# Kernel optimization log

Hardware: AMD Instinct MI355X
Metric: run time of the kernel (lower is better)

The kernel has to match this reference:

```python
import jax, jax.numpy as jnp
import numpy as np

B, T, C, H = 4, 2048, 1024, 16
HD = C // H  # head_dim = 64


def _rope(x, cos, sin):
    # x: [B,H,T,HD]; cos/sin: [T,HD//2] -> broadcast [1,1,T,HD//2]
    x1 = x[..., 0::2]
    x2 = x[..., 1::2]
    cos = cos[None, None]
    sin = sin[None, None]
    o1 = x1 * cos - x2 * sin
    o2 = x1 * sin + x2 * cos
    # interleave back to [..., HD]
    return jnp.stack([o1, o2], axis=-1).reshape(x.shape)


def setup_inputs() -> dict:
    key = jax.random.key(0)
    ks = jax.random.split(key, 10)
    x = jax.random.normal(ks[0], (B, T, C), jnp.float32)
    # rotary frequencies (llama-style, theta=10000), stored as (cos,sin)
    inv_freq = 1.0 / (10000.0 ** (jnp.arange(0, HD, 2, dtype=jnp.float32) / HD))
    freqs = jnp.outer(jnp.arange(T, dtype=jnp.float32), inv_freq)  # [T, HD/2]
    freqs_cis = jnp.stack([jnp.cos(freqs), jnp.sin(freqs)], axis=-1)  # [T, HD/2, 2]
    attn_mask = jnp.tril(jnp.ones((T, T), jnp.int32))  # causal
    padding_mask = jnp.ones((B, T), jnp.int32)
    w = 0.02
    Wq = jax.random.normal(ks[1], (C, C), jnp.float32) * w
    Wk = jax.random.normal(ks[2], (C, C), jnp.float32) * w
    Wv = jax.random.normal(ks[3], (C, C), jnp.float32) * w
    Wp = jax.random.normal(ks[4], (C, C), jnp.float32) * w
    bq = jnp.zeros((C,), jnp.float32)
    bk = jnp.zeros((C,), jnp.float32)
    bv = jnp.zeros((C,), jnp.float32)
    bp = jnp.zeros((C,), jnp.float32)
    return {"x": x, "freqs_cis": freqs_cis, "attn_mask": attn_mask,
            "padding_mask": padding_mask, "Wq": Wq, "bq": bq, "Wk": Wk,
            "bk": bk, "Wv": Wv, "bv": bv, "Wp": Wp, "bp": bp}


def reference(x, freqs_cis, attn_mask, padding_mask, Wq, bq, Wk, bk, Wv, bv, Wp, bp):
    b, t, c = x.shape
    # qkv projections -> [B,H,T,HD]
    def heads(y):
        return y.reshape(b, t, H, HD).transpose(0, 2, 1, 3)
    q = heads(x @ Wq.T + bq)
    k = heads(x @ Wk.T + bk)
    v = heads(x @ Wv.T + bv)
    cos, sin = freqs_cis[..., 0], freqs_cis[..., 1]  # [T, HD/2]
    q = _rope(q, cos, sin)
    k = _rope(k, cos, sin)
    att = jnp.einsum('bhqd,bhkd->bhqk', q, k) * (1.0 / np.sqrt(HD).astype(np.float32))
    att = jnp.where(attn_mask[None, None] == 0, -1e30, att)
    att = jnp.where(padding_mask[:, None, None, :] == 0, -1e30, att)
    att = jax.nn.softmax(att, axis=-1)
    # dropout omitted (eval mode / deterministic reference)
    y = jnp.einsum('bhqk,bhkd->bhqd', att, v)
    y = y.transpose(0, 2, 1, 3).reshape(b, t, c)
    return y @ Wp.T + bp
```

## Files before the change

kernel.cpp:

```cpp
#include <hip/hip_runtime.h>
#include <hip/hip_bf16.h>

#define TB 2048
#define CC 1024
#define NH 16
#define HD 64
#define NB 4
#define BHX (NB*NH)
#define BTX (NB*TB)
#define NITEMS 2048

typedef __attribute__((ext_vector_type(8))) short bf16x8;
typedef __attribute__((ext_vector_type(4))) float f32x4;
typedef __attribute__((ext_vector_type(4))) unsigned short us4;

__device__ __forceinline__ unsigned short bfb(float f) {
  __hip_bfloat16 h = __float2bfloat16(f);
  return __builtin_bit_cast(unsigned short, h);
}
__device__ __forceinline__ float fexp2(float x) {
  return __builtin_amdgcn_exp2f(x);
}
template <int CTRL>
__device__ __forceinline__ float dppf(float x) {
  int r = __builtin_amdgcn_update_dpp(0, __builtin_bit_cast(int, x), CTRL, 0xf, 0xf, false);
  return __builtin_bit_cast(float, r);
}

__device__ __forceinline__ void gld_lds16(const void* g, void* l) {
  __builtin_amdgcn_global_load_lds(
      (const __attribute__((address_space(1))) unsigned*)g,
      (__attribute__((address_space(3))) unsigned*)l, 16, 0, 0);
}

__global__ void cvt_f32_bf16(const float* __restrict__ src,
                             unsigned short* __restrict__ dst, int n4) {
  int i = blockIdx.x * blockDim.x + threadIdx.x;
  if (i >= n4) return;
  f32x4 v = ((const f32x4*)src)[i];
  us4 o;
#pragma unroll
  for (int j = 0; j < 4; j++) o[j] = bfb(v[j]);
  ((us4*)dst)[i] = o;
}

__global__ void cvt_w4(const float* __restrict__ s0, const float* __restrict__ s1,
                       const float* __restrict__ s2, const float* __restrict__ s3,
                       unsigned short* __restrict__ d0, unsigned short* __restrict__ d1,
                       unsigned short* __restrict__ d2, unsigned short* __restrict__ d3) {
  int y = blockIdx.y;
  const float* s = y == 0 ? s0 : y == 1 ? s1 : y == 2 ? s2 : s3;
  unsigned short* d = y == 0 ? d0 : y == 1 ? d1 : y == 2 ? d2 : d3;
  int i = blockIdx.x * 256 + threadIdx.x;
  f32x4 v = ((const f32x4*)s)[i];
  us4 o;
#pragma unroll
  for (int j = 0; j < 4; j++) o[j] = bfb(v[j]);
  ((us4*)d)[i] = o;
}

__global__ void prep_bias(const float* __restrict__ bq, const float* __restrict__ bk,
                          const float* __restrict__ bv, float* __restrict__ out) {
  int i = blockIdx.x * 256 + threadIdx.x;
  float v = i < 1024 ? bq[i] : i < 2048 ? bk[i - 1024] : bv[i - 2048];
  out[i] = v;
}

template <int MODE>
__global__ __launch_bounds__(256) void gemm_bt(
    const unsigned short* __restrict__ A, const unsigned short* __restrict__ Bw,
    const float* __restrict__ bias, const float* __restrict__ fcg,
    void* __restrict__ Cout, int M, int N, int K)
{
  __shared__ __align__(16) unsigned short As[128 * 32];
  __shared__ __align__(16) unsigned short Bs[128 * 32];
  int tid = threadIdx.x;
  int lane = tid & 63, wid = tid >> 6;
  int g = lane >> 4, l4 = lane & 15;
  int wr = wid >> 1, wc = wid & 1;
  int brow = blockIdx.y * 128, bcol = blockIdx.x * 128;

  const unsigned short* ap = A + (size_t)(brow + (tid >> 2)) * K + (tid & 3) * 8;
  const unsigned short* bp_ = Bw + (size_t)(bcol + (tid >> 2)) * K + (tid & 3) * 8;
  const size_t rstep = (size_t)64 * K;
  unsigned short* asl = As + tid * 8;
  unsigned short* bsl = Bs + tid * 8;

  f32x4 acc[4][4] = {};

  for (int k0 = 0; k0 < K; k0 += 32) {
    gld_lds16(ap, asl);
    gld_lds16(ap + rstep, asl + 2048);
    gld_lds16(bp_, bsl);
    gld_lds16(bp_ + rstep, bsl + 2048);
    ap += 32; bp_ += 32;
    __syncthreads();
    bf16x8 af[4], bfr[4];
#pragma unroll
    for (int i = 0; i < 4; i++)
      af[i] = *(const bf16x8*)&As[(wr * 64 + i * 16 + l4) * 32 + g * 8];
#pragma unroll
    for (int i = 0; i < 4; i++)
      bfr[i] = *(const bf16x8*)&Bs[(wc * 64 + i * 16 + l4) * 32 + g * 8];
#pragma unroll
    for (int i = 0; i < 4; i++)
#pragma unroll
      for (int j = 0; j < 4; j++)
        acc[i][j] = __builtin_amdgcn_mfma_f32_16x16x32_bf16(af[i], bfr[j], acc[i][j], 0, 0, 0);
    __syncthreads();
  }

#pragma unroll
  for (int i = 0; i < 4; i++) {
    int grow0 = brow + wr * 64 + i * 16 + 4 * g;
#pragma unroll
    for (int j = 0; j < 4; j++) {
      int gcol = bcol + wc * 64 + j * 16 + l4;
      float bv = bias[gcol];
      if (MODE == 0) {
        float* out = (float*)Cout;
#pragma unroll
        for (int r = 0; r < 4; r++)
          out[(size_t)(grow0 + r) * N + gcol] = acc[i][j][r] + bv;
      } else {
        unsigned short* out = (unsigned short*)Cout;
        int part = gcol >> 10;
        int c = gcol & 1023;
        int h = c >> 6, d = c & 63;
        int dbase = d & ~1;
        float sgn = (d & 1) ? 1.f : -1.f;
        bool isqk = (part < 2);
#pragma unroll
        for (int r = 0; r < 4; r++) {
          int grow = grow0 + r;
          int b = grow >> 11, t = grow & 2047;
          float v = acc[i][j][r] + bv;
          float w = __shfl_xor(v, 1, 64);
          float o = v;
          if (isqk) {
            float cth = fcg[(size_t)t * 64 + dbase];
            float sth = fcg[(size_t)t * 64 + dbase + 1];
            o = v * cth + sgn * w * sth;
          }
          size_t dst = (size_t)part * ((size_t)BHX * TB * HD)
                     + ((size_t)(b * NH + h) * TB + t) * HD + d;
          out[dst] = bfb(o);
        }
      }
    }
  }
}

__global__ void transpose_v(const unsigned short* __restrict__ v,
                            unsigned short* __restrict__ vT) {
  int bh = blockIdx.y, t0 = blockIdx.x * 64;
  __shared__ __align__(16) unsigned short tile[64][72];
  int tid = threadIdx.x;
#pragma unroll
  for (int s = 0; s < 2; s++) {
    int cid = tid + 256 * s;
    int r = cid >> 3, c8 = (cid & 7) * 8;
    bf16x8 val = *(const bf16x8*)(v + ((size_t)bh * TB + t0 + r) * HD + c8);
    *(bf16x8*)&tile[r][c8] = val;
  }
  __syncthreads();
#pragma unroll
  for (int s = 0; s < 2; s++) {
    int cid = tid + 256 * s;
    int rr = cid >> 3, cc = (cid & 7) * 8;
    bf16x8 o;
#pragma unroll
    for (int i = 0; i < 8; i++) o[i] = (short)tile[cc + i][rr];
    *(bf16x8*)(vT + ((size_t)bh * HD + rr) * TB + t0 + cc) = o;
  }
}

__global__ __launch_bounds__(256, 4) void flash_fwd(
    const unsigned short* __restrict__ q, const unsigned short* __restrict__ k,
    const unsigned short* __restrict__ vT, unsigned short* __restrict__ yb,
    int* __restrict__ ctr)
{
  __shared__ __align__(16) unsigned short Ks[2][4096];
  __shared__ __align__(16) unsigned short Vs[2][4096];
  __shared__ __align__(16) unsigned short Ps[4][16][64];

  const int tid = threadIdx.x, wid = tid >> 6, lane = tid & 63;
  const int g = lane >> 4, l4 = lane & 15;

  const int off0 = tid << 4;
  const int row0 = off0 >> 7, sc0 = ((off0 >> 4) & 7) ^ (row0 & 7);
  const int off1 = off0 + 4096;
  const int row1 = off1 >> 7, sc1 = ((off1 >> 4) & 7) ^ (row1 & 7);
  const int koff0 = (row0 << 6) + (sc0 << 3);
  const int koff1 = (row1 << 6) + (sc1 << 3);
  const int voff0 = (row0 << 11) + (sc0 << 3);
  const int voff1 = (row1 << 11) + (sc1 << 3);

  const float SCL2 = 0.18033688011112042f;

  for (;;) {
    __syncthreads();
    if (tid == 0) *(int*)&Ps[0][0][0] = atomicAdd(ctr, 1);
    __syncthreads();
    const int w = *(const int*)&Ps[0][0][0];
    if (w >= NITEMS) break;
    const int q64 = 31 - (w >> 6), bh = w & 63;
    const int rbase = q64 * 64 + wid * 16;

    const unsigned short* kb = k  + ((size_t)bh << 17);
    const unsigned short* vb = vT + ((size_t)bh << 17);

    bf16x8 qf0, qf1;
    {
      const unsigned short* qp = q + (((size_t)bh * TB + rbase + l4) << 6);
      qf0 = *(const bf16x8*)(qp + g * 8);
      qf1 = *(const bf16x8*)(qp + 32 + g * 8);
    }

    float m_run[4], l_run[4];
    f32x4 acc_o[4] = {};
#pragma unroll
    for (int j = 0; j < 4; j++) { m_run[j] = -1e30f; l_run[j] = 0.f; }

    gld_lds16(kb + koff0, &Ks[0][off0 >> 1]);
    gld_lds16(kb + koff1, &Ks[0][off1 >> 1]);
    gld_lds16(vb + voff0, &Vs[0][off0 >> 1]);
    gld_lds16(vb + voff1, &Vs[0][off1 >> 1]);
    __syncthreads();

    for (int kt = 0; kt <= q64; kt++) {
      const int cur = kt & 1;
      if (kt < q64) {
        const int kadd = (kt + 1) << 12;
        const int vadd = (kt + 1) << 6;
        gld_lds16(kb + koff0 + kadd, &Ks[cur ^ 1][off0 >> 1]);
        gld_lds16(kb + koff1 + kadd, &Ks[cur ^ 1][off1 >> 1]);
        gld_lds16(vb + voff0 + vadd, &Vs[cur ^ 1][off0 >> 1]);
        gld_lds16(vb + voff1 + vadd, &Vs[cur ^ 1][off1 >> 1]);
      }
      const unsigned short* Kc = Ks[cur];
      const unsigned short* Vc = Vs[cur];

      float sv[4][4];
      __builtin_amdgcn_s_setprio(1);
#pragma unroll
      for (int cb = 0; cb < 4; cb++) {
        const int r = cb * 16 + l4;
        const int sw = (r & 7) * 8;
        bf16x8 kb0 = *(const bf16x8*)&Kc[r * 64 + ((g * 8) ^ sw)];
        bf16x8 kb1 = *(const bf16x8*)&Kc[r * 64 + (((g + 4) * 8) ^ sw)];
        f32x4 z = {0.f, 0.f, 0.f, 0.f};
        z = __builtin_amdgcn_mfma_f32_16x16x32_bf16(qf0, kb0, z, 0, 0, 0);
        z = __builtin_amdgcn_mfma_f32_16x16x32_bf16(qf1, kb1, z, 0, 0, 0);
#pragma unroll
        for (int j = 0; j < 4; j++)
          sv[cb][j] = z[j] * SCL2;
      }
      __builtin_amdgcn_s_setprio(0);
      if (kt == q64) {
        const int rq = wid * 16 + 4 * g;
#pragma unroll
        for (int cb = 0; cb < 4; cb++)
#pragma unroll
          for (int j = 0; j < 4; j++)
            if (cb * 16 + l4 > rq + j) sv[cb][j] = -1e30f;
      }

      float mt[4];
#pragma unroll
      for (int j = 0; j < 4; j++) {
        float m = fmaxf(fmaxf(sv[0][j], sv[1][j]), fmaxf(sv[2][j], sv[3][j]));
        m = fmaxf(m, dppf<0x121>(m));
        m = fmaxf(m, dppf<0x122>(m));
        m = fmaxf(m, dppf<0x124>(m));
        m = fmaxf(m, dppf<0x128>(m));
        mt[j] = m;
      }
      bool need = !((mt[0] <= m_run[0] + 8.f) & (mt[1] <= m_run[1] + 8.f) &
                    (mt[2] <= m_run[2] + 8.f) & (mt[3] <= m_run[3] + 8.f));
      if (__any(need)) {
#pragma unroll
        for (int j = 0; j < 4; j++) {
          float mn = fmaxf(m_run[j], mt[j]);
          float alpha = fexp2(m_run[j] - mn);
          m_run[j] = mn;
          l_run[j] *= alpha;
#pragma unroll
          for (int db = 0; db < 4; db++) acc_o[db][j] *= alpha;
        }
      }
#pragma unroll
      for (int j = 0; j < 4; j++) {
        float s0 = fexp2(sv[0][j] - m_run[j]); sv[0][j] = s0;
        float s1 = fexp2(sv[1][j] - m_run[j]); sv[1][j] = s1;
        float s2 = fexp2(sv[2][j] - m_run[j]); sv[2][j] = s2;
        float s3 = fexp2(sv[3][j] - m_run[j]); sv[3][j] = s3;
        float p = (s0 + s1) + (s2 + s3);
        p += dppf<0x121>(p);
        p += dppf<0x122>(p);
        p += dppf<0x124>(p);
        p += dppf<0x128>(p);
        l_run[j] += p;
      }

#pragma unroll
      for (int cb = 0; cb < 4; cb++)
#pragma unroll
        for (int j = 0; j < 4; j++) {
          const int xch = (cb * 2 + (l4 >> 3)) ^ ((g & 1) * 4 + j);
          Ps[wid][4 * g + j][xch * 8 + (l4 & 7)] = bfb(sv[cb][j]);
        }
      asm volatile("s_waitcnt lgkmcnt(0)" ::: "memory");
      __builtin_amdgcn_sched_barrier(0);
      bf16x8 pa0 = *(const bf16x8*)&Ps[wid][l4][(g ^ (l4 & 7)) * 8];
      bf16x8 pa1 = *(const bf16x8*)&Ps[wid][l4][((4 + g) ^ (l4 & 7)) * 8];
      __builtin_amdgcn_s_setprio(1);
#pragma unroll
      for (int db = 0; db < 4; db++) {
        const int r = db * 16 + l4;
        const int sw = (r & 7) * 8;
        bf16x8 vb0 = *(const bf16x8*)&Vc[r * 64 + ((g * 8) ^ sw)];
        bf16x8 vb1 = *(const bf16x8*)&Vc[r * 64 + (((g + 4) * 8) ^ sw)];
        acc_o[db] = __builtin_amdgcn_mfma_f32_16x16x32_bf16(pa0, vb0, acc_o[db], 0, 0, 0);
        acc_o[db] = __builtin_amdgcn_mfma_f32_16x16x32_bf16(pa1, vb1, acc_o[db], 0, 0, 0);
      }
      __builtin_amdgcn_s_setprio(0);
      __syncthreads();
    }

    unsigned short* yp = yb + ((size_t)(bh >> 4) * TB) * CC + (size_t)(bh & 15) * HD;
    const int qr0 = rbase + 4 * g;
    float inv[4];
#pragma unroll
    for (int j = 0; j < 4; j++) inv[j] = 1.0f / l_run[j];
#pragma unroll
    for (int db = 0; db < 4; db++) {
      const int d = db * 16 + l4;
#pragma unroll
      for (int j = 0; j < 4; j++)
        yp[(size_t)(qr0 + j) * CC + d] = bfb(acc_o[db][j] * inv[j]);
    }
  }
}

extern "C" void kernel_launch(void* const* d_in, const int* in_sizes, int n_in,
                              void* d_out, int out_size, void* d_ws, size_t ws_size,
                              hipStream_t stream) {
  (void)in_sizes; (void)n_in; (void)out_size; (void)ws_size;
  const float* x  = (const float*)d_in[0];
  const float* fc = (const float*)d_in[1];
  const float* Wq = (const float*)d_in[4];
  const float* bq = (const float*)d_in[5];
  const float* Wk = (const float*)d_in[6];
  const float* bk = (const float*)d_in[7];
  const float* Wv = (const float*)d_in[8];
  const float* bv = (const float*)d_in[9];
  const float* Wp = (const float*)d_in[10];
  const float* bp = (const float*)d_in[11];

  char* ws = (char*)d_ws;
  unsigned short* xb   = (unsigned short*)(ws + 0);
  unsigned short* wqkv = (unsigned short*)(ws + 16777216);
  unsigned short* wp   = (unsigned short*)(ws + 23068672);
  float*          bqkv = (float*)(ws + 25165824);
  int*            ctr  = (int*)(ws + 25178112);
  unsigned short* qkv  = (unsigned short*)(ws + 25182208);
  unsigned short* vT   = qkv + 3 * (size_t)8388608;
  unsigned short* yb   = xb;

  cvt_f32_bf16<<<(2097152 + 255) / 256, 256, 0, stream>>>(x, xb, 2097152);
  cvt_w4<<<dim3(1024, 4), 256, 0, stream>>>(Wq, Wk, Wv, Wp,
      wqkv, wqkv + 1048576, wqkv + 2097152, wp);
  prep_bias<<<dim3(12), 256, 0, stream>>>(bq, bk, bv, bqkv);
  (void)hipMemsetAsync(ctr, 0, 4, stream);

  gemm_bt<1><<<dim3(24, 64), 256, 0, stream>>>(xb, wqkv, bqkv, fc, qkv, BTX, 3072, 1024);
  transpose_v<<<dim3(32, 64), 256, 0, stream>>>(qkv + 2 * (size_t)8388608, vT);
  flash_fwd<<<dim3(1024), 256, 0, stream>>>(qkv, qkv + (size_t)8388608, vT, yb, ctr);
  gemm_bt<0><<<dim3(8, 64), 256, 0, stream>>>(yb, wp, bp, nullptr, (float*)d_out, BTX, 1024, 1024);
}
```

Measured before the change: 246.6 us.

## Partition flash attention work queue per XCD with global work-stealing fallback

Replaces the single global atomic work counter with per-XCD counters, so each XCD first processes items whose heads map to it (bh low bits from the XCD id). K/V for those heads then stay in that XCD's L2. Once a local queue is exhausted, blocks steal from a global counter, and a claimed-flag array prevents duplicate work. This adds more atomics per item and a larger memset. The item order within each XCD still runs the longest causal rows first.

```diff
diff --git a/kernel.cpp b/kernel.cpp
--- a/kernel.cpp
+++ b/kernel.cpp
@@ -178,7 +178,7 @@
 __global__ __launch_bounds__(256, 4) void flash_fwd(
     const unsigned short* __restrict__ q, const unsigned short* __restrict__ k,
     const unsigned short* __restrict__ vT, unsigned short* __restrict__ yb,
-    int* __restrict__ ctr)
+    int* __restrict__ ctrs, int* __restrict__ claimed)
 {
   __shared__ __align__(16) unsigned short Ks[2][4096];
   __shared__ __align__(16) unsigned short Vs[2][4096];
@@ -186,6 +186,10 @@
 
   const int tid = threadIdx.x, wid = tid >> 6, lane = tid & 63;
   const int g = lane >> 4, l4 = lane & 15;
+
+  int xcd;
+  asm("s_getreg_b32 %0, hwreg(HW_REG_XCC_ID)" : "=s"(xcd));
+  xcd &= 7;
 
   const int off0 = tid << 4;
   const int row0 = off0 >> 7, sc0 = ((off0 >> 4) & 7) ^ (row0 & 7);
@@ -198,13 +202,34 @@
 
   const float SCL2 = 0.18033688011112042f;
 
+  bool own = true;
   for (;;) {
     __syncthreads();
-    if (tid == 0) *(int*)&Ps[0][0][0] = atomicAdd(ctr, 1);
+    if (tid == 0) {
+      int item;
+      if (own) {
+        int it = atomicAdd(&ctrs[xcd], 1);
+        if (it < 256) {
+          item = (xcd << 8) | it;
+          if (atomicExch(&claimed[item], 1)) item = -3;
+        } else item = -2;
+      } else {
+        item = -1;
+        for (;;) {
+          int it = atomicAdd(&ctrs[8], 1);
+          if (it >= NITEMS) break;
+          if (atomicExch(&claimed[it], 1) == 0) { item = it; break; }
+        }
+      }
+      *(int*)&Ps[0][0][0] = item;
+    }
     __syncthreads();
-    const int w = *(const int*)&Ps[0][0][0];
-    if (w >= NITEMS) break;
-    const int q64 = 31 - (w >> 6), bh = w & 63;
+    const int item = *(const int*)&Ps[0][0][0];
+    if (item == -3) continue;
+    if (item == -2) { own = false; continue; }
+    if (item < 0) break;
+    const int bh = ((item >> 8) << 3) | (item & 7);
+    const int q64 = 31 - ((item >> 3) & 31);
     const int rbase = q64 * 64 + wid * 16;
 
     const unsigned short* kb = k  + ((size_t)bh << 17);
@@ -363,19 +388,20 @@
   unsigned short* wqkv = (unsigned short*)(ws + 16777216);
   unsigned short* wp   = (unsigned short*)(ws + 23068672);
   float*          bqkv = (float*)(ws + 25165824);
-  int*            ctr  = (int*)(ws + 25178112);
   unsigned short* qkv  = (unsigned short*)(ws + 25182208);
   unsigned short* vT   = qkv + 3 * (size_t)8388608;
+  int*            claimed = (int*)(ws + 92291072);
+  int*            ctrs = (int*)(ws + 92299264);
   unsigned short* yb   = xb;
 
   cvt_f32_bf16<<<(2097152 + 255) / 256, 256, 0, stream>>>(x, xb, 2097152);
   cvt_w4<<<dim3(1024, 4), 256, 0, stream>>>(Wq, Wk, Wv, Wp,
       wqkv, wqkv + 1048576, wqkv + 2097152, wp);
   prep_bias<<<dim3(12), 256, 0, stream>>>(bq, bk, bv, bqkv);
-  (void)hipMemsetAsync(ctr, 0, 4, stream);
+  (void)hipMemsetAsync(claimed, 0, 8192 + 64, stream);
 
   gemm_bt<1><<<dim3(24, 64), 256, 0, stream>>>(xb, wqkv, bqkv, fc, qkv, BTX, 3072, 1024);
   transpose_v<<<dim3(32, 64), 256, 0, stream>>>(qkv + 2 * (size_t)8388608, vT);
-  flash_fwd<<<dim3(1024), 256, 0, stream>>>(qkv, qkv + (size_t)8388608, vT, yb, ctr);
+  flash_fwd<<<dim3(1024), 256, 0, stream>>>(qkv, qkv + (size_t)8388608, vT, yb, ctrs, claimed);
   gemm_bt<0><<<dim3(8, 64), 256, 0, stream>>>(yb, wp, bp, nullptr, (float*)d_out, BTX, 1024, 1024);
 }
```

Measured after the change: 279.3 us. 13.3% more time.

## Replace atomic work queue with static paired causal tiles and XCD-aware head mapping

Applied to the files above, without the earlier changes.

The flash attention kernel no longer pulls work items from a global atomic counter. Each of the 1024 blocks now handles two query tiles of one (batch, head), tile p and tile 31-p, so causal work is balanced per block. Heads are assigned so that blocks on the same XCD (blockIdx mod 8) share K/V of the same heads, which is meant to improve L2 reuse. This also drops the per-item atomic, the extra barriers and the memset, at the cost of losing dynamic load balancing.

```diff
diff --git a/kernel.cpp b/kernel.cpp
--- a/kernel.cpp
+++ b/kernel.cpp
@@ -8,7 +8,6 @@
 #define NB 4
 #define BHX (NB*NH)
 #define BTX (NB*TB)
-#define NITEMS 2048
 
 typedef __attribute__((ext_vector_type(8))) short bf16x8;
 typedef __attribute__((ext_vector_type(4))) float f32x4;
@@ -177,8 +176,7 @@
 
 __global__ __launch_bounds__(256, 4) void flash_fwd(
     const unsigned short* __restrict__ q, const unsigned short* __restrict__ k,
-    const unsigned short* __restrict__ vT, unsigned short* __restrict__ yb,
-    int* __restrict__ ctr)
+    const unsigned short* __restrict__ vT, unsigned short* __restrict__ yb)
 {
   __shared__ __align__(16) unsigned short Ks[2][4096];
   __shared__ __align__(16) unsigned short Vs[2][4096];
@@ -186,6 +184,12 @@
 
   const int tid = threadIdx.x, wid = tid >> 6, lane = tid & 63;
   const int g = lane >> 4, l4 = lane & 15;
+
+  const int b = blockIdx.x;
+  const int xcd = b & 7;
+  const int idx = b >> 3;
+  const int bh = (xcd << 3) | (idx & 7);
+  const int p = idx >> 3;
 
   const int off0 = tid << 4;
   const int row0 = off0 >> 7, sc0 = ((off0 >> 4) & 7) ^ (row0 & 7);
@@ -198,17 +202,13 @@
 
   const float SCL2 = 0.18033688011112042f;
 
-  for (;;) {
-    __syncthreads();
-    if (tid == 0) *(int*)&Ps[0][0][0] = atomicAdd(ctr, 1);
-    __syncthreads();
-    const int w = *(const int*)&Ps[0][0][0];
-    if (w >= NITEMS) break;
-    const int q64 = 31 - (w >> 6), bh = w & 63;
+  const unsigned short* kb = k  + ((size_t)bh << 17);
+  const unsigned short* vb = vT + ((size_t)bh << 17);
+
+#pragma unroll 1
+  for (int sel = 0; sel < 2; sel++) {
+    const int q64 = sel ? (31 - p) : p;
     const int rbase = q64 * 64 + wid * 16;
-
-    const unsigned short* kb = k  + ((size_t)bh << 17);
-    const unsigned short* vb = vT + ((size_t)bh << 17);
 
     bf16x8 qf0, qf1;
     {
@@ -295,12 +295,12 @@
         float s1 = fexp2(sv[1][j] - m_run[j]); sv[1][j] = s1;
         float s2 = fexp2(sv[2][j] - m_run[j]); sv[2][j] = s2;
         float s3 = fexp2(sv[3][j] - m_run[j]); sv[3][j] = s3;
-        float p = (s0 + s1) + (s2 + s3);
-        p += dppf<0x121>(p);
-        p += dppf<0x122>(p);
-        p += dppf<0x124>(p);
-        p += dppf<0x128>(p);
-        l_run[j] += p;
+        float p2 = (s0 + s1) + (s2 + s3);
+        p2 += dppf<0x121>(p2);
+        p2 += dppf<0x122>(p2);
+        p2 += dppf<0x124>(p2);
+        p2 += dppf<0x128>(p2);
+        l_run[j] += p2;
       }
 
 #pragma unroll
@@ -363,7 +363,6 @@
   unsigned short* wqkv = (unsigned short*)(ws + 16777216);
   unsigned short* wp   = (unsigned short*)(ws + 23068672);
   float*          bqkv = (float*)(ws + 25165824);
-  int*            ctr  = (int*)(ws + 25178112);
   unsigned short* qkv  = (unsigned short*)(ws + 25182208);
   unsigned short* vT   = qkv + 3 * (size_t)8388608;
   unsigned short* yb   = xb;
@@ -372,10 +371,9 @@
   cvt_w4<<<dim3(1024, 4), 256, 0, stream>>>(Wq, Wk, Wv, Wp,
       wqkv, wqkv + 1048576, wqkv + 2097152, wp);
   prep_bias<<<dim3(12), 256, 0, stream>>>(bq, bk, bv, bqkv);
-  (void)hipMemsetAsync(ctr, 0, 4, stream);
 
   gemm_bt<1><<<dim3(24, 64), 256, 0, stream>>>(xb, wqkv, bqkv, fc, qkv, BTX, 3072, 1024);
   transpose_v<<<dim3(32, 64), 256, 0, stream>>>(qkv + 2 * (size_t)8388608, vT);
-  flash_fwd<<<dim3(1024), 256, 0, stream>>>(qkv, qkv + (size_t)8388608, vT, yb, ctr);
+  flash_fwd<<<dim3(1024), 256, 0, stream>>>(qkv, qkv + (size_t)8388608, vT, yb);
   gemm_bt<0><<<dim3(8, 64), 256, 0, stream>>>(yb, wp, bp, nullptr, (float*)d_out, BTX, 1024, 1024);
 }
```

Measured after the change: 234.1 us. -5.1%, faster.
